# Optimization experiments

Hardware: AMD Instinct MI355X
Metric: run time of the kernel (lower is better)

Reference implementation:

```python
import jax, jax.numpy as jnp
import numpy as np

B, S, D, H, M, E, K = 4, 2048, 1024, 2048, 64, 8, 2  # batch, seq, d_model, max_neurons, moe_hidden, experts, top_k


def setup_inputs() -> dict:
    key = jax.random.key(0)
    ks = jax.random.split(key, 10)
    r = lambda k, shape: jax.random.normal(k, shape, dtype=jnp.float32) * 0.02
    return {
        "inputs_embeds": jax.random.normal(ks[0], (B, S, D), dtype=jnp.float32),
        "enc_W": r(ks[1], (D, H)), "enc_b": jnp.zeros((H,), jnp.float32),
        "s2c_W": r(ks[2], (H, M)), "s2c_b": jnp.zeros((M,), jnp.float32),
        "rW1": r(ks[3], (M, 64)), "rb1": jnp.zeros((64,), jnp.float32),
        "rW2": r(ks[4], (64, E)), "rb2": jnp.zeros((E,), jnp.float32),
        "We1": r(ks[5], (E, M, H // 2)), "be1": jnp.zeros((E, H // 2), jnp.float32),
        "We2": r(ks[6], (E, H // 2, M)), "be2": jnp.zeros((E, M), jnp.float32),
        "c2s_W": r(ks[7], (M, H)), "c2s_b": jnp.zeros((H,), jnp.float32),
        "dec_W": r(ks[8], (H, D)), "dec_b": jnp.zeros((D,), jnp.float32),
        "ln_g": jnp.ones((D,), jnp.float32), "ln_b": jnp.zeros((D,), jnp.float32),
    }


def _layernorm(x, g, b, eps=1e-5):
    mu = x.mean(-1, keepdims=True)
    var = ((x - mu) ** 2).mean(-1, keepdims=True)
    return (x - mu) * jax.lax.rsqrt(var + eps) * g + b


def _forward(inputs_embeds, enc_W, enc_b, s2c_W, s2c_b, rW1, rb1, rW2, rb2,
             We1, be1, We2, be2, c2s_W, c2s_b, dec_W, dec_b, ln_g, ln_b):
    b, s, _ = inputs_embeds.shape
    # GIFNeuron encoder (rate-coded surrogate spikes)
    spikes_enc = jax.nn.sigmoid(inputs_embeds @ enc_W + enc_b)          # (B,S,H)
    flat = spikes_enc.reshape(b * s, H)                                  # (N,H)
    # SpikeToContinuousBridge ('rate'): projection to MoE hidden
    cont = flat @ s2c_W + s2c_b                                          # (N,M)
    # LiquidMoERouter: 2-layer router, softmax, top-k, renormalize
    logits = jnp.tanh(cont @ rW1 + rb1) @ rW2 + rb2                      # (N,E)
    probs = jax.nn.softmax(logits, axis=-1)
    topw, topi = jax.lax.top_k(probs, K)                                 # (N,K)
    w = topw / topw.sum(-1, keepdims=True)
    # dense per-token per-expert gate == sum_k weights[:,k] * (indices[:,k]==e)
    gates = (jax.nn.one_hot(topi, E, dtype=cont.dtype) * w[..., None]).sum(1)  # (N,E)
    # SNNExpert MLP per expert, dense dispatch + weighted combine (index_add equivalent)
    h = jax.nn.relu(jnp.einsum('nm,emh->enh', cont, We1) + be1[:, None, :])    # (E,N,H/2)
    expert_out = jnp.einsum('enh,ehm->enm', h, We2) + be2[:, None, :]          # (E,N,M)
    output_flat = jnp.einsum('enm,ne->nm', expert_out, gates)                  # (N,M)
    # ContinuousToSpikeBridge ('poisson', expected rate), 2D -> 1 timestep
    spikes_moe = jax.nn.sigmoid(output_flat @ c2s_W + c2s_b).reshape(b, s, H)
    # GIFNeuron decoder + LayerNorm
    decoded = jax.nn.sigmoid(spikes_moe @ dec_W + dec_b)                 # (B,S,D)
    return _layernorm(decoded, ln_g, ln_b)


def reference(inputs_embeds, enc_W, enc_b, s2c_W, s2c_b, rW1, rb1, rW2, rb2,
              We1, be1, We2, be2, c2s_W, c2s_b, dec_W, dec_b, ln_g, ln_b):
    return _forward(inputs_embeds, enc_W, enc_b, s2c_W, s2c_b, rW1, rb1, rW2, rb2,
                    We1, be1, We2, be2, c2s_W, c2s_b, dec_W, dec_b, ln_g, ln_b)
```

## Files before the change

### kernel.cpp

```cpp
#include <hip/hip_runtime.h>
#include <hip/hip_bf16.h>
#include <cstdint>
#include <cstddef>

#define TOK    8192
#define DMODEL 1024
#define HDIM   2048
#define MDIM   64
#define NEXP   8
#define HHALF  1024

using f32x4  = __attribute__((ext_vector_type(4))) float;
using bf16x8 = __attribute__((ext_vector_type(8))) __bf16;
using bf16x4 = __attribute__((ext_vector_type(4))) __bf16;

__device__ __forceinline__ void async16(const void* g, void* l) {
  __builtin_amdgcn_global_load_lds(
      (const __attribute__((address_space(1))) unsigned int*)g,
      (__attribute__((address_space(3))) unsigned int*)l, 16, 0, 0);
}

__global__ __launch_bounds__(256) void preamble_kernel(
    const float* __restrict__ X, __bf16* __restrict__ Xb,
    const float* __restrict__ encW, __bf16* __restrict__ encWT,
    const float* __restrict__ s2cW, __bf16* __restrict__ s2cWT,
    const float* __restrict__ c2sW, __bf16* __restrict__ c2sWT,
    const float* __restrict__ decW, __bf16* __restrict__ decWT,
    const float* __restrict__ We1, __bf16* __restrict__ We1T,
    const float* __restrict__ We2, __bf16* __restrict__ We2T) {
  __shared__ float ts[32][33];
  const int tid = threadIdx.x;
  int b = blockIdx.x;
  if (b < 8192) {
    int i = b * 256 + tid;
    float4 v = ((const float4*)X)[i];
    bf16x4 o = { (__bf16)v.x, (__bf16)v.y, (__bf16)v.z, (__bf16)v.w };
    ((bf16x4*)Xb)[i] = o;
    return;
  }
  b -= 8192;
  const float* in; __bf16* outp; int R, C, tx, ty;
  if (b < 2048)              { in = encW; outp = encWT; R = 1024; C = 2048; tx = b % 64; ty = b / 64; }
  else if ((b -= 2048) < 128){ in = s2cW; outp = s2cWT; R = 2048; C = 64;   tx = b % 2;  ty = b / 2;  }
  else if ((b -= 128) < 128) { in = c2sW; outp = c2sWT; R = 64;   C = 2048; tx = b % 64; ty = b / 64; }
  else if ((b -= 128) < 2048){ in = decW; outp = decWT; R = 2048; C = 1024; tx = b % 32; ty = b / 32; }
  else if ((b -= 2048) < 512){ int s = b / 64, t = b % 64;
                               in = We1 + (size_t)s * 65536; outp = We1T + (size_t)s * 65536;
                               R = 64; C = 1024; tx = t % 32; ty = t / 32; }
  else                       { b -= 512; int s = b / 64, t = b % 64;
                               in = We2 + (size_t)s * 65536; outp = We2T + (size_t)s * 65536;
                               R = 1024; C = 64; tx = t % 2; ty = t / 2; }
  const int c0 = tx * 32, r0 = ty * 32;
  const int x = tid & 31, y = tid >> 5;
  #pragma unroll
  for (int i = y; i < 32; i += 8) ts[i][x] = in[(size_t)(r0 + i) * C + c0 + x];
  __syncthreads();
  #pragma unroll
  for (int i = y; i < 32; i += 8)
    outp[(size_t)(c0 + i) * R + r0 + x] = (__bf16)ts[x][i];
}
#define PREAMBLE_BLOCKS (8192 + 2048 + 128 + 128 + 2048 + 512 + 512)

template <int BN, int WAVES, int NBUF, int OUT_BF16, int ACT, int BIAS>
__global__ __launch_bounds__(WAVES * 64, 2) void gemm_mt(
    const __bf16* __restrict__ A, const __bf16* __restrict__ Bt,
    const float* __restrict__ bias, void* __restrict__ Cout,
    int M, int N, int K) {
  constexpr int BM = 256, BK = 64;
  constexpr int A_ISSUES = BM / (8 * WAVES);
  constexpr int B_ISSUES = BN / (8 * WAVES);
  constexpr int LOADS = A_ISSUES + B_ISSUES;
  static_assert(NBUF == 2 && LOADS == 8, "vmcnt literal assumes LOADS=8");
  __shared__ __bf16 As[NBUF * BM * BK];
  __shared__ __bf16 Bs[NBUF * BN * BK];
  const int tid = threadIdx.x;
  const int wave = tid >> 6, lane = tid & 63;
  const int quad = lane >> 4, l16 = lane & 15;
  const int m0 = blockIdx.x * BM, n0 = blockIdx.y * BN;
  const int wm = (wave & 1) * 128;
  const int wn = (wave >> 1) * 64;
  const int lrow = lane >> 3, lchunk = lane & 7;
  f32x4 acc[8][4] = {};

  const __bf16* aSrc[A_ISSUES];
  const __bf16* bSrc[B_ISSUES];
  #pragma unroll
  for (int t = 0; t < A_ISSUES; ++t) {
    int row = (t * WAVES + wave) * 8 + lrow;
    aSrc[t] = A + (size_t)(m0 + row) * K + (lchunk ^ (row & 7)) * 8;
  }
  #pragma unroll
  for (int t = 0; t < B_ISSUES; ++t) {
    int row = (t * WAVES + wave) * 8 + lrow;
    bSrc[t] = Bt + (size_t)(n0 + row) * K + (lchunk ^ (row & 7)) * 8;
  }
  int aOff[8], bOff[4];
  #pragma unroll
  for (int rf = 0; rf < 8; ++rf) {
    int row = wm + rf * 16 + l16;
    aOff[rf] = row * BK + ((quad ^ (row & 7)) * 8);
  }
  #pragma unroll
  for (int cf = 0; cf < 4; ++cf) {
    int row = wn + cf * 16 + l16;
    bOff[cf] = row * BK + ((quad ^ (row & 7)) * 8);
  }

  auto stage = [&](__bf16* Ad, __bf16* Bd) {
    #pragma unroll
    for (int t = 0; t < A_ISSUES; ++t) {
      async16(aSrc[t], Ad + (t * WAVES + wave) * 8 * BK);
      aSrc[t] += BK;
    }
    #pragma unroll
    for (int t = 0; t < B_ISSUES; ++t) {
      async16(bSrc[t], Bd + (t * WAVES + wave) * 8 * BK);
      bSrc[t] += BK;
    }
  };

  __bf16 *cA0 = As, *cA1 = As + BM * BK;
  __bf16 *cB0 = Bs, *cB1 = Bs + BN * BK;
  const int nt = K / BK;
  stage(cA0, cB0);

  for (int t = 0; t < nt; ++t) {
    if (t + 1 < nt) stage(cA1, cB1);
    if (t + 1 < nt) asm volatile("s_waitcnt vmcnt(8)" ::: "memory");
    else            asm volatile("s_waitcnt vmcnt(0)" ::: "memory");
    asm volatile("s_barrier" ::: "memory");

    bf16x8 af[4], ag[4], bv[4], bw[4];
    #pragma unroll
    for (int r = 0; r < 4; ++r) af[r] = *(const bf16x8*)(cA0 + aOff[r]);
    #pragma unroll
    for (int c = 0; c < 4; ++c) bv[c] = *(const bf16x8*)(cB0 + bOff[c]);
    #pragma unroll
    for (int r = 0; r < 4; ++r) ag[r] = *(const bf16x8*)(cA0 + aOff[4 + r]);
    __builtin_amdgcn_s_setprio(1);
    #pragma unroll
    for (int c = 0; c < 4; ++c)
      #pragma unroll
      for (int r = 0; r < 4; ++r)
        acc[r][c] = __builtin_amdgcn_mfma_f32_16x16x32_bf16(af[r], bv[c], acc[r][c], 0, 0, 0);
    __builtin_amdgcn_s_setprio(0);
    asm volatile("s_barrier" ::: "memory");
    #pragma unroll
    for (int r = 0; r < 4; ++r) af[r] = *(const bf16x8*)(cA0 + (aOff[r] ^ 32));
    #pragma unroll
    for (int c = 0; c < 4; ++c) bw[c] = *(const bf16x8*)(cB0 + (bOff[c] ^ 32));
    __builtin_amdgcn_s_setprio(1);
    #pragma unroll
    for (int c = 0; c < 4; ++c)
      #pragma unroll
      for (int r = 0; r < 4; ++r)
        acc[4 + r][c] = __builtin_amdgcn_mfma_f32_16x16x32_bf16(ag[r], bv[c], acc[4 + r][c], 0, 0, 0);
    __builtin_amdgcn_s_setprio(0);
    asm volatile("s_barrier" ::: "memory");
    #pragma unroll
    for (int r = 0; r < 4; ++r) ag[r] = *(const bf16x8*)(cA0 + (aOff[4 + r] ^ 32));
    __builtin_amdgcn_s_setprio(1);
    #pragma unroll
    for (int c = 0; c < 4; ++c)
      #pragma unroll
      for (int r = 0; r < 4; ++r)
        acc[r][c] = __builtin_amdgcn_mfma_f32_16x16x32_bf16(af[r], bw[c], acc[r][c], 0, 0, 0);
    __builtin_amdgcn_s_setprio(0);
    asm volatile("s_barrier" ::: "memory");
    __builtin_amdgcn_s_setprio(1);
    #pragma unroll
    for (int c = 0; c < 4; ++c)
      #pragma unroll
      for (int r = 0; r < 4; ++r)
        acc[4 + r][c] = __builtin_amdgcn_mfma_f32_16x16x32_bf16(ag[r], bw[c], acc[4 + r][c], 0, 0, 0);
    __builtin_amdgcn_s_setprio(0);
    asm volatile("s_barrier" ::: "memory");

    __bf16* x;
    x = cA0; cA0 = cA1; cA1 = x;
    x = cB0; cB0 = cB1; cB1 = x;
  }

  #pragma unroll
  for (int rf = 0; rf < 8; ++rf)
    #pragma unroll
    for (int cf = 0; cf < 4; ++cf)
      #pragma unroll
      for (int r = 0; r < 4; ++r) {
        int m = m0 + wm + rf * 16 + quad * 4 + r;
        int n = n0 + wn + cf * 16 + l16;
        float v = acc[rf][cf][r];
        if (BIAS) v += bias[n];
        if (ACT == 1) v = 1.0f / (1.0f + __expf(-v));
        if (OUT_BF16)
          ((__bf16*)Cout)[(size_t)m * N + n] = (__bf16)v;
        else
          ((float*)Cout)[(size_t)m * N + n] = v;
      }
}

template <int BM, int BN, int WAVES, int OUT_BF16, int ACT, int BIAS, int SUMA>
__global__ __launch_bounds__(WAVES * 64) void gemm_bt(
    const __bf16* __restrict__ A, const __bf16* __restrict__ Bt,
    const float* __restrict__ bias, void* __restrict__ Cout,
    int M, int N, int K, const __bf16* __restrict__ A2) {
  constexpr int BK = 64;
  constexpr int WAVES_N = WAVES / 2;
  constexpr int WTM = BM / 32;
  constexpr int WTN = BN / (WAVES_N * 16);
  constexpr int NBUF = SUMA ? 1 : 2;
  constexpr int A_ISSUES = BM / (8 * WAVES);
  constexpr int B_ISSUES = BN / (8 * WAVES);
  __shared__ __bf16 As[NBUF * BM * BK];
  __shared__ __bf16 Bs[NBUF * BN * BK];
  const int tid = threadIdx.x;
  const int wave = tid >> 6, lane = tid & 63;
  const int quad = lane >> 4, l16 = lane & 15;
  const int m0 = blockIdx.x * BM, n0 = blockIdx.y * BN;
  const int ks = K / gridDim.z;
  const int kbeg = blockIdx.z * ks;
  const int wm = (wave & 1) * (BM / 2);
  const int wn = (wave >> 1) * (BN / WAVES_N);
  const int lrow = lane >> 3;
  const int lchunk = lane & 7;
  f32x4 acc[WTM][WTN] = {};

  const __bf16* aSrc[A_ISSUES];
  const __bf16* bSrc[B_ISSUES];
  #pragma unroll
  for (int t = 0; t < A_ISSUES; ++t) {
    int row = (t * WAVES + wave) * 8 + lrow;
    aSrc[t] = A + (size_t)(m0 + row) * K + kbeg + (lchunk ^ (row & 7)) * 8;
  }
  #pragma unroll
  for (int t = 0; t < B_ISSUES; ++t) {
    int row = (t * WAVES + wave) * 8 + lrow;
    bSrc[t] = Bt + (size_t)(n0 + row) * K + kbeg + (lchunk ^ (row & 7)) * 8;
  }
  int aOff[WTM][2], bOff[WTN][2];
  #pragma unroll
  for (int i = 0; i < WTM; ++i) {
    int row = wm + i * 16 + l16;
    #pragma unroll
    for (int kk = 0; kk < 2; ++kk)
      aOff[i][kk] = row * BK + (((kk * 4 + quad) ^ (row & 7)) * 8);
  }
  #pragma unroll
  for (int j = 0; j < WTN; ++j) {
    int row = wn + j * 16 + l16;
    #pragma unroll
    for (int kk = 0; kk < 2; ++kk)
      bOff[j][kk] = row * BK + (((kk * 4 + quad) ^ (row & 7)) * 8);
  }

  auto stage = [&](__bf16* Ad, __bf16* Bd) {
    #pragma unroll
    for (int t = 0; t < A_ISSUES; ++t) {
      async16(aSrc[t], Ad + (t * WAVES + wave) * 8 * BK);
      aSrc[t] += BK;
    }
    #pragma unroll
    for (int t = 0; t < B_ISSUES; ++t) {
      async16(bSrc[t], Bd + (t * WAVES + wave) * 8 * BK);
      bSrc[t] += BK;
    }
  };
  auto compute = [&](const __bf16* Ab, const __bf16* Bb) {
    #pragma unroll
    for (int kk = 0; kk < 2; ++kk) {
      bf16x8 af[WTM], bfr[WTN];
      #pragma unroll
      for (int i = 0; i < WTM; ++i) af[i] = *(const bf16x8*)(Ab + aOff[i][kk]);
      #pragma unroll
      for (int j = 0; j < WTN; ++j) bfr[j] = *(const bf16x8*)(Bb + bOff[j][kk]);
      #pragma unroll
      for (int i = 0; i < WTM; ++i)
        #pragma unroll
        for (int j = 0; j < WTN; ++j)
          acc[i][j] = __builtin_amdgcn_mfma_f32_16x16x32_bf16(af[i], bfr[j], acc[i][j], 0, 0, 0);
    }
  };

  const int niter = ks / BK;
  if constexpr (SUMA) {
    for (int it = 0; it < niter; ++it) {
      __syncthreads();
      #pragma unroll
      for (int t = 0; t < A_ISSUES; ++t) {
        int row = (t * WAVES + wave) * 8 + lrow;
        size_t go = (size_t)(m0 + row) * K + kbeg + it * BK + lchunk * 8;
        bf16x8 a0 = *(const bf16x8*)(A + go);
        bf16x8 a1 = *(const bf16x8*)(A2 + go);
        bf16x8 s;
        #pragma unroll
        for (int q = 0; q < 8; ++q) s[q] = (__bf16)((float)a0[q] + (float)a1[q]);
        *(bf16x8*)(As + row * BK + ((lchunk ^ (row & 7)) * 8)) = s;
      }
      #pragma unroll
      for (int t = 0; t < B_ISSUES; ++t) {
        async16(bSrc[t], Bs + (t * WAVES + wave) * 8 * BK);
        bSrc[t] += BK;
      }
      __syncthreads();
      compute(As, Bs);
    }
  } else {
    __bf16* curA = As;  __bf16* nxtA = As + BM * BK;
    __bf16* curB = Bs;  __bf16* nxtB = Bs + BN * BK;
    stage(curA, curB);
    asm volatile("s_waitcnt vmcnt(0)" ::: "memory");
    __builtin_amdgcn_s_barrier();
    for (int it = 0; it < niter - 1; ++it) {
      stage(nxtA, nxtB);
      compute(curA, curB);
      asm volatile("s_waitcnt vmcnt(0)" ::: "memory");
      __builtin_amdgcn_s_barrier();
      { __bf16* t = curA; curA = nxtA; nxtA = t; }
      { __bf16* t = curB; curB = nxtB; nxtB = t; }
    }
    compute(curA, curB);
  }

  char* Cz = (char*)Cout + (size_t)blockIdx.z * M * N * (OUT_BF16 ? 2 : 4);
  #pragma unroll
  for (int i = 0; i < WTM; ++i)
    #pragma unroll
    for (int j = 0; j < WTN; ++j)
      #pragma unroll
      for (int r = 0; r < 4; ++r) {
        int m = m0 + wm + i * 16 + quad * 4 + r;
        int n = n0 + wn + j * 16 + l16;
        float v = acc[i][j][r];
        if (BIAS) v += bias[n];
        if (ACT == 1) v = 1.0f / (1.0f + __expf(-v));
        if (OUT_BF16)
          ((__bf16*)Cz)[(size_t)m * N + n] = (__bf16)v;
        else
          ((float*)Cz)[(size_t)m * N + n] = v;
      }
}

__global__ __launch_bounds__(256) void router_kernel(
    const float* __restrict__ contP, const float* __restrict__ s2c_b,
    const float* __restrict__ rW1, const float* __restrict__ rb1,
    const float* __restrict__ rW2, const float* __restrict__ rb2,
    __bf16* __restrict__ contB, int* __restrict__ e01,
    float2* __restrict__ g01, int* __restrict__ cnt) {
  if (blockIdx.x == 0 && threadIdx.x < NEXP) cnt[threadIdx.x] = 0;
  const int wave = threadIdx.x >> 6, lane = threadIdx.x & 63;
  const int n = blockIdx.x * 4 + wave;
  const size_t base = (size_t)n * 64 + lane;
  const size_t slab = (size_t)TOK * 64;
  float c = contP[base] + contP[base + slab] + contP[base + 2 * slab] +
            contP[base + 3 * slab] + s2c_b[lane];
  contB[base] = (__bf16)c;
  float acc = rb1[lane];
  #pragma unroll
  for (int i = 0; i < 64; ++i) {
    float ci = __shfl(c, i);
    acc = fmaf(ci, rW1[i * 64 + lane], acc);
  }
  float t = tanhf(acc);
  float logit[8];
  #pragma unroll
  for (int e = 0; e < 8; ++e) {
    float v = t * rW2[lane * 8 + e];
    #pragma unroll
    for (int o = 32; o; o >>= 1) v += __shfl_xor(v, o);
    logit[e] = v + rb2[e];
  }
  float mx = logit[0];
  #pragma unroll
  for (int e = 1; e < 8; ++e) mx = fmaxf(mx, logit[e]);
  float p[8];
  #pragma unroll
  for (int e = 0; e < 8; ++e) p[e] = __expf(logit[e] - mx);
  float v0 = p[0]; int e0 = 0;
  #pragma unroll
  for (int e = 1; e < 8; ++e) if (p[e] > v0) { v0 = p[e]; e0 = e; }
  float v1 = -1.0f; int e1 = 0;
  #pragma unroll
  for (int e = 0; e < 8; ++e) if (e != e0 && p[e] > v1) { v1 = p[e]; e1 = e; }
  float inv = 1.0f / (v0 + v1);
  if (lane == 0) {
    e01[n] = e0 | (e1 << 8);
    g01[n] = make_float2(v0 * inv, v1 * inv);
  }
}

__global__ __launch_bounds__(256) void fill_kernel(
    const int* __restrict__ e01, int* __restrict__ cnt,
    unsigned* __restrict__ idxb) {
  __shared__ int lcnt[NEXP], lbase[NEXP];
  const int tid = threadIdx.x;
  if (tid < NEXP) lcnt[tid] = 0;
  __syncthreads();
  const int n = blockIdx.x * 256 + tid;
  const int pe = e01[n];
  const int e0 = pe & 0xff, e1 = (pe >> 8) & 0xff;
  const int p0 = atomicAdd(&lcnt[e0], 1);
  const int p1 = atomicAdd(&lcnt[e1], 1);
  __syncthreads();
  if (tid < NEXP) lbase[tid] = atomicAdd(&cnt[tid], lcnt[tid]);
  __syncthreads();
  idxb[e0 * TOK + lbase[e0] + p0] = (unsigned)n;
  idxb[e1 * TOK + lbase[e1] + p1] = (unsigned)n | 0x80000000u;
}

__global__ __launch_bounds__(256) void moe_sparse_kernel(
    const __bf16* __restrict__ contB, const __bf16* __restrict__ We1T,
    const __bf16* __restrict__ We2T, const float* __restrict__ be1,
    const float* __restrict__ be2, const unsigned* __restrict__ idxb,
    const int* __restrict__ cnt, const float2* __restrict__ g01,
    __bf16* __restrict__ slab0, __bf16* __restrict__ slab1) {
  constexpr int TT = 64;
  const int e = blockIdx.y;
  const int start = blockIdx.x * TT;
  const int ne = cnt[e];
  if (start >= ne) return;
  const int nval = min(TT, ne - start);
  __shared__ __bf16 cont_s[TT * 64];
  __shared__ __bf16 w1_s[64 * 64];
  __shared__ __bf16 w2_s[64 * 64];
  __shared__ __bf16 h_s[TT * 64];
  __shared__ unsigned tok_s[TT];
  __shared__ float gate_s[TT];
  const int tid = threadIdx.x;
  const int wave = tid >> 6, lane = tid & 63;
  const int quad = lane >> 4, l16 = lane & 15;
  if (tid < TT) {
    unsigned v = idxb[e * TOK + start + ((tid < nval) ? tid : 0)];
    unsigned tok = v & 0x7fffffffu;
    float2 g = g01[tok];
    tok_s[tid] = v;
    gate_s[tid] = (v >> 31) ? g.y : g.x;
  }
  __syncthreads();
  for (int i = tid; i < TT * 8; i += 256) {
    int r = i >> 3, cc = i & 7;
    unsigned tok = tok_s[r] & 0x7fffffffu;
    *(uint4*)(cont_s + r * 64 + ((cc ^ (r & 7)) * 8)) =
        *(const uint4*)(contB + (size_t)tok * 64 + cc * 8);
  }
  const int wtok = wave * 16;
  f32x4 acc2[4] = {};
  for (int hc = 0; hc < HHALF; hc += 64) {
    __syncthreads();
    for (int c = tid; c < 512; c += 256) {
      int r = c >> 3, cc = c & 7;
      *(uint4*)(w1_s + r * 64 + ((cc ^ (r & 7)) * 8)) =
          *(const uint4*)(We1T + ((size_t)e * HHALF + hc + r) * 64 + cc * 8);
      *(uint4*)(w2_s + r * 64 + ((cc ^ (r & 7)) * 8)) =
          *(const uint4*)(We2T + ((size_t)e * 64 + r) * HHALF + hc + cc * 8);
    }
    __syncthreads();
    f32x4 acc1[4] = {};
    #pragma unroll
    for (int kk = 0; kk < 2; ++kk) {
      bf16x8 af, bfr[4];
      {
        int row = wtok + l16;
        af = *(const bf16x8*)(cont_s + row * 64 + (((kk * 4 + quad) ^ (row & 7)) * 8));
      }
      #pragma unroll
      for (int j = 0; j < 4; ++j) {
        int row = j * 16 + l16;
        bfr[j] = *(const bf16x8*)(w1_s + row * 64 + (((kk * 4 + quad) ^ (row & 7)) * 8));
      }
      #pragma unroll
      for (int j = 0; j < 4; ++j)
        acc1[j] = __builtin_amdgcn_mfma_f32_16x16x32_bf16(af, bfr[j], acc1[j], 0, 0, 0);
    }
    #pragma unroll
    for (int j = 0; j < 4; ++j)
      #pragma unroll
      for (int r = 0; r < 4; ++r) {
        int tr = wtok + quad * 4 + r;
        int hcol = j * 16 + l16;
        float v = acc1[j][r] + be1[e * HHALF + hc + hcol];
        h_s[tr * 64 + (((hcol >> 3) ^ (tr & 7)) * 8) + (hcol & 7)] =
            (__bf16)fmaxf(v, 0.0f);
      }
    #pragma unroll
    for (int kk = 0; kk < 2; ++kk) {
      bf16x8 af, bfr[4];
      {
        int row = wtok + l16;
        af = *(const bf16x8*)(h_s + row * 64 + (((kk * 4 + quad) ^ (row & 7)) * 8));
      }
      #pragma unroll
      for (int j = 0; j < 4; ++j) {
        int row = j * 16 + l16;
        bfr[j] = *(const bf16x8*)(w2_s + row * 64 + (((kk * 4 + quad) ^ (row & 7)) * 8));
      }
      #pragma unroll
      for (int j = 0; j < 4; ++j)
        acc2[j] = __builtin_amdgcn_mfma_f32_16x16x32_bf16(af, bfr[j], acc2[j], 0, 0, 0);
    }
  }
  #pragma unroll
  for (int j = 0; j < 4; ++j)
    #pragma unroll
    for (int r = 0; r < 4; ++r) {
      int tr = wtok + quad * 4 + r;
      if (tr < nval) {
        unsigned v = tok_s[tr];
        unsigned tok = v & 0x7fffffffu;
        int m = j * 16 + l16;
        float o = gate_s[tr] * (acc2[j][r] + be2[e * 64 + m]);
        __bf16* slab = (v >> 31) ? slab1 : slab0;
        slab[(size_t)tok * 64 + m] = (__bf16)o;
      }
    }
}

__global__ __launch_bounds__(256) void ln_kernel(
    const float* __restrict__ x, const float* __restrict__ g,
    const float* __restrict__ b, float* __restrict__ out) {
  const int row = blockIdx.x;
  const float4 v = ((const float4*)(x + (size_t)row * 1024))[threadIdx.x];
  float s1 = v.x + v.y + v.z + v.w;
  float s2 = v.x * v.x + v.y * v.y + v.z * v.z + v.w * v.w;
  #pragma unroll
  for (int o = 32; o; o >>= 1) { s1 += __shfl_xor(s1, o); s2 += __shfl_xor(s2, o); }
  __shared__ float ws1[4], ws2[4];
  const int wave = threadIdx.x >> 6, lane = threadIdx.x & 63;
  if (lane == 0) { ws1[wave] = s1; ws2[wave] = s2; }
  __syncthreads();
  s1 = ws1[0] + ws1[1] + ws1[2] + ws1[3];
  s2 = ws2[0] + ws2[1] + ws2[2] + ws2[3];
  const float mu = s1 * (1.0f / 1024.0f);
  const float var = s2 * (1.0f / 1024.0f) - mu * mu;
  const float inv = rsqrtf(var + 1e-5f);
  const int col = threadIdx.x * 4;
  const float4 gv = *(const float4*)(g + col);
  const float4 bv = *(const float4*)(b + col);
  float4 o;
  o.x = (v.x - mu) * inv * gv.x + bv.x;
  o.y = (v.y - mu) * inv * gv.y + bv.y;
  o.z = (v.z - mu) * inv * gv.z + bv.z;
  o.w = (v.w - mu) * inv * gv.w + bv.w;
  *(float4*)(out + (size_t)row * 1024 + col) = o;
}

extern "C" void kernel_launch(void* const* d_in, const int* in_sizes, int n_in,
                              void* d_out, int out_size, void* d_ws, size_t ws_size,
                              hipStream_t stream) {
  const float* X     = (const float*)d_in[0];
  const float* enc_W = (const float*)d_in[1];
  const float* enc_b = (const float*)d_in[2];
  const float* s2c_W = (const float*)d_in[3];
  const float* s2c_b = (const float*)d_in[4];
  const float* rW1   = (const float*)d_in[5];
  const float* rb1   = (const float*)d_in[6];
  const float* rW2   = (const float*)d_in[7];
  const float* rb2   = (const float*)d_in[8];
  const float* We1   = (const float*)d_in[9];
  const float* be1   = (const float*)d_in[10];
  const float* We2   = (const float*)d_in[11];
  const float* be2   = (const float*)d_in[12];
  const float* c2s_W = (const float*)d_in[13];
  const float* c2s_b = (const float*)d_in[14];
  const float* dec_W = (const float*)d_in[15];
  const float* dec_b = (const float*)d_in[16];
  const float* ln_g  = (const float*)d_in[17];
  const float* ln_b  = (const float*)d_in[18];
  float* out = (float*)d_out;

  char* ws = (char*)d_ws;
  size_t off = 0;
  auto take = [&](size_t bytes) -> char* {
    char* p = ws + off;
    off = (off + bytes + 255) & ~(size_t)255;
    return p;
  };
  const size_t SLAB = (size_t)TOK * HDIM * 2;
  char*   slabA     = take(SLAB);
  char*   slabB     = take(SLAB);
  __bf16* encWT     = (__bf16*)take((size_t)HDIM * DMODEL * 2);
  __bf16* s2cWT     = (__bf16*)take((size_t)MDIM * HDIM * 2);
  __bf16* c2sWT     = (__bf16*)take((size_t)HDIM * MDIM * 2);
  __bf16* decWT     = (__bf16*)take((size_t)DMODEL * HDIM * 2);
  __bf16* We1T      = (__bf16*)take((size_t)NEXP * HHALF * MDIM * 2);
  __bf16* We2T      = (__bf16*)take((size_t)NEXP * MDIM * HHALF * 2);
  __bf16* contB     = (__bf16*)take((size_t)TOK * MDIM * 2);
  int*    e01       = (int*)take((size_t)TOK * 4);
  float2* g01       = (float2*)take((size_t)TOK * 8);
  __bf16* oslab0    = (__bf16*)take((size_t)TOK * MDIM * 2);
  __bf16* oslab1    = (__bf16*)take((size_t)TOK * MDIM * 2);
  int*     cnt      = (int*)take((size_t)NEXP * 4);
  unsigned* idxb    = (unsigned*)take((size_t)NEXP * TOK * 4);
  if (off > ws_size) return;

  __bf16* Xb        = (__bf16*)slabA;
  float*  contP     = (float*)(slabA + (size_t)TOK * DMODEL * 2);
  __bf16* spikesMoe = (__bf16*)slabA;
  __bf16* spikesEnc = (__bf16*)slabB;
  float*  decoded   = (float*)slabB;

  preamble_kernel<<<PREAMBLE_BLOCKS, 256, 0, stream>>>(
      X, Xb, enc_W, encWT, s2c_W, s2cWT, c2s_W, c2sWT, dec_W, decWT,
      We1, We1T, We2, We2T);

  gemm_mt<256, 8, 2, 1, 1, 1><<<dim3(TOK / 256, HDIM / 256), 512, 0, stream>>>(
      Xb, encWT, enc_b, spikesEnc, TOK, HDIM, DMODEL);
  gemm_bt<128, 64, 4, 0, 0, 0, 0><<<dim3(TOK / 128, 1, 4), 256, 0, stream>>>(
      spikesEnc, s2cWT, nullptr, contP, TOK, MDIM, HDIM, nullptr);
  router_kernel<<<TOK / 4, 256, 0, stream>>>(contP, s2c_b, rW1, rb1, rW2, rb2,
                                             contB, e01, g01, cnt);
  fill_kernel<<<TOK / 256, 256, 0, stream>>>(e01, cnt, idxb);
  moe_sparse_kernel<<<dim3(TOK / 64, NEXP), 256, 0, stream>>>(
      contB, We1T, We2T, be1, be2, idxb, cnt, g01, oslab0, oslab1);
  gemm_bt<128, 128, 4, 1, 1, 1, 1><<<dim3(TOK / 128, HDIM / 128, 1), 256, 0, stream>>>(
      oslab0, c2sWT, c2s_b, spikesMoe, TOK, HDIM, MDIM, oslab1);
  gemm_bt<128, 128, 4, 0, 1, 1, 0><<<dim3(TOK / 128, DMODEL / 128, 1), 256, 0, stream>>>(
      spikesMoe, decWT, dec_b, decoded, TOK, DMODEL, HDIM, nullptr);
  ln_kernel<<<TOK, 256, 0, stream>>>(decoded, ln_g, ln_b, out);
}
```

Before: 311.7 us.

## Interleave next-tile async loads across MFMA phases and reuse kernel for decoder GEMM

The 8-wave 256-row GEMM now issues the next K-tile's global-to-LDS loads in chunks between the four MFMA phases instead of all at once at the top of each iteration. The goal is to overlap memory traffic with compute and smooth out VMEM issue. The kernel is generalized to BN=128 and also used for the decoder GEMM, which replaces the 128x128 4-wave gemm_bt. This adds scheduling barriers and hand-tuned vmcnt waits whose correctness depends on the exact load counts per phase.

```diff
diff --git a/kernel.cpp b/kernel.cpp
--- a/kernel.cpp
+++ b/kernel.cpp
@@ -61,130 +61,161 @@
 }
 #define PREAMBLE_BLOCKS (8192 + 2048 + 128 + 128 + 2048 + 512 + 512)
 
-template <int BN, int WAVES, int NBUF, int OUT_BF16, int ACT, int BIAS>
-__global__ __launch_bounds__(WAVES * 64, 2) void gemm_mt(
+template <int BN, int OUT_BF16, int ACT, int BIAS>
+__global__ __launch_bounds__(512, 2) void gemm_8p(
     const __bf16* __restrict__ A, const __bf16* __restrict__ Bt,
     const float* __restrict__ bias, void* __restrict__ Cout,
     int M, int N, int K) {
   constexpr int BM = 256, BK = 64;
-  constexpr int A_ISSUES = BM / (8 * WAVES);
-  constexpr int B_ISSUES = BN / (8 * WAVES);
-  constexpr int LOADS = A_ISSUES + B_ISSUES;
-  static_assert(NBUF == 2 && LOADS == 8, "vmcnt literal assumes LOADS=8");
-  __shared__ __bf16 As[NBUF * BM * BK];
-  __shared__ __bf16 Bs[NBUF * BN * BK];
+  constexpr int WTN = BN / 64;
+  constexpr int A_LOADS = 4;
+  constexpr int B_LOADS = BN / 64;
+  __shared__ __bf16 As[2 * BM * BK];
+  __shared__ __bf16 Bs[2 * BN * BK];
   const int tid = threadIdx.x;
   const int wave = tid >> 6, lane = tid & 63;
   const int quad = lane >> 4, l16 = lane & 15;
   const int m0 = blockIdx.x * BM, n0 = blockIdx.y * BN;
   const int wm = (wave & 1) * 128;
-  const int wn = (wave >> 1) * 64;
+  const int wn = (wave >> 1) * (BN / 4);
   const int lrow = lane >> 3, lchunk = lane & 7;
-  f32x4 acc[8][4] = {};
-
-  const __bf16* aSrc[A_ISSUES];
-  const __bf16* bSrc[B_ISSUES];
-  #pragma unroll
-  for (int t = 0; t < A_ISSUES; ++t) {
-    int row = (t * WAVES + wave) * 8 + lrow;
+  f32x4 acc[8][WTN] = {};
+
+  const __bf16* aSrc[A_LOADS];
+  const __bf16* bSrc[B_LOADS];
+  #pragma unroll
+  for (int t = 0; t < A_LOADS; ++t) {
+    int row = (t * 8 + wave) * 8 + lrow;
     aSrc[t] = A + (size_t)(m0 + row) * K + (lchunk ^ (row & 7)) * 8;
   }
   #pragma unroll
-  for (int t = 0; t < B_ISSUES; ++t) {
-    int row = (t * WAVES + wave) * 8 + lrow;
+  for (int t = 0; t < B_LOADS; ++t) {
+    int row = (t * 8 + wave) * 8 + lrow;
     bSrc[t] = Bt + (size_t)(n0 + row) * K + (lchunk ^ (row & 7)) * 8;
   }
-  int aOff[8], bOff[4];
+  int aOff[8], bOff[WTN];
   #pragma unroll
   for (int rf = 0; rf < 8; ++rf) {
     int row = wm + rf * 16 + l16;
     aOff[rf] = row * BK + ((quad ^ (row & 7)) * 8);
   }
   #pragma unroll
-  for (int cf = 0; cf < 4; ++cf) {
+  for (int cf = 0; cf < WTN; ++cf) {
     int row = wn + cf * 16 + l16;
     bOff[cf] = row * BK + ((quad ^ (row & 7)) * 8);
   }
 
-  auto stage = [&](__bf16* Ad, __bf16* Bd) {
-    #pragma unroll
-    for (int t = 0; t < A_ISSUES; ++t) {
-      async16(aSrc[t], Ad + (t * WAVES + wave) * 8 * BK);
-      aSrc[t] += BK;
-    }
-    #pragma unroll
-    for (int t = 0; t < B_ISSUES; ++t) {
-      async16(bSrc[t], Bd + (t * WAVES + wave) * 8 * BK);
-      bSrc[t] += BK;
-    }
+  auto stageA = [&](int t, __bf16* Ad) {
+    async16(aSrc[t], Ad + (t * 8 + wave) * 8 * BK);
+    aSrc[t] += BK;
   };
-
-  __bf16 *cA0 = As, *cA1 = As + BM * BK;
-  __bf16 *cB0 = Bs, *cB1 = Bs + BN * BK;
+  auto stageB = [&](int t, __bf16* Bd) {
+    async16(bSrc[t], Bd + (t * 8 + wave) * 8 * BK);
+    bSrc[t] += BK;
+  };
+
+  __bf16 *curA = As, *nxtA = As + BM * BK;
+  __bf16 *curB = Bs, *nxtB = Bs + BN * BK;
   const int nt = K / BK;
-  stage(cA0, cB0);
+
+  stageB(0, curB); stageB(1, curB);
+  if constexpr (BN == 256) { stageB(2, curB); stageB(3, curB); }
+  stageA(0, curA); stageA(2, curA);
+  stageA(1, curA); stageA(3, curA);
+  asm volatile("s_waitcnt vmcnt(0)" ::: "memory");
+  __builtin_amdgcn_s_barrier();
 
   for (int t = 0; t < nt; ++t) {
-    if (t + 1 < nt) stage(cA1, cB1);
-    if (t + 1 < nt) asm volatile("s_waitcnt vmcnt(8)" ::: "memory");
-    else            asm volatile("s_waitcnt vmcnt(0)" ::: "memory");
-    asm volatile("s_barrier" ::: "memory");
-
-    bf16x8 af[4], ag[4], bv[4], bw[4];
-    #pragma unroll
-    for (int r = 0; r < 4; ++r) af[r] = *(const bf16x8*)(cA0 + aOff[r]);
-    #pragma unroll
-    for (int c = 0; c < 4; ++c) bv[c] = *(const bf16x8*)(cB0 + bOff[c]);
-    #pragma unroll
-    for (int r = 0; r < 4; ++r) ag[r] = *(const bf16x8*)(cA0 + aOff[4 + r]);
+    const bool pre = (t + 1 < nt);
+    bf16x8 af[4], bv[WTN];
+    #pragma unroll
+    for (int r = 0; r < 4; ++r) af[r] = *(const bf16x8*)(curA + aOff[r]);
+    #pragma unroll
+    for (int c = 0; c < WTN; ++c) bv[c] = *(const bf16x8*)(curB + bOff[c]);
+    if (pre) {
+      stageB(0, nxtB); stageB(1, nxtB);
+      asm volatile("s_waitcnt vmcnt(2)" ::: "memory");
+    } else {
+      asm volatile("s_waitcnt vmcnt(0)" ::: "memory");
+    }
+    __builtin_amdgcn_s_barrier();
+    __builtin_amdgcn_sched_barrier(0);
     __builtin_amdgcn_s_setprio(1);
     #pragma unroll
-    for (int c = 0; c < 4; ++c)
+    for (int c = 0; c < WTN; ++c)
       #pragma unroll
       for (int r = 0; r < 4; ++r)
         acc[r][c] = __builtin_amdgcn_mfma_f32_16x16x32_bf16(af[r], bv[c], acc[r][c], 0, 0, 0);
     __builtin_amdgcn_s_setprio(0);
-    asm volatile("s_barrier" ::: "memory");
-    #pragma unroll
-    for (int r = 0; r < 4; ++r) af[r] = *(const bf16x8*)(cA0 + (aOff[r] ^ 32));
-    #pragma unroll
-    for (int c = 0; c < 4; ++c) bw[c] = *(const bf16x8*)(cB0 + (bOff[c] ^ 32));
+    __builtin_amdgcn_s_barrier();
+    bf16x8 ag[4];
+    #pragma unroll
+    for (int r = 0; r < 4; ++r) ag[r] = *(const bf16x8*)(curA + aOff[4 + r]);
+    if (pre) {
+      if constexpr (BN == 256) { stageB(2, nxtB); stageB(3, nxtB); }
+      else                     { stageA(0, nxtA); stageA(2, nxtA); }
+    }
+    __builtin_amdgcn_s_barrier();
+    __builtin_amdgcn_sched_barrier(0);
     __builtin_amdgcn_s_setprio(1);
     #pragma unroll
-    for (int c = 0; c < 4; ++c)
+    for (int c = 0; c < WTN; ++c)
       #pragma unroll
       for (int r = 0; r < 4; ++r)
         acc[4 + r][c] = __builtin_amdgcn_mfma_f32_16x16x32_bf16(ag[r], bv[c], acc[4 + r][c], 0, 0, 0);
     __builtin_amdgcn_s_setprio(0);
-    asm volatile("s_barrier" ::: "memory");
-    #pragma unroll
-    for (int r = 0; r < 4; ++r) ag[r] = *(const bf16x8*)(cA0 + (aOff[4 + r] ^ 32));
+    __builtin_amdgcn_s_barrier();
+    bf16x8 af2[4], bw[WTN];
+    #pragma unroll
+    for (int r = 0; r < 4; ++r) af2[r] = *(const bf16x8*)(curA + (aOff[r] ^ 32));
+    #pragma unroll
+    for (int c = 0; c < WTN; ++c) bw[c] = *(const bf16x8*)(curB + (bOff[c] ^ 32));
+    if (pre) {
+      if constexpr (BN == 256) { stageA(0, nxtA); stageA(2, nxtA); }
+      else {
+        stageA(1, nxtA); stageA(3, nxtA);
+        asm volatile("s_waitcnt vmcnt(2)" ::: "memory");
+      }
+    }
+    __builtin_amdgcn_s_barrier();
+    __builtin_amdgcn_sched_barrier(0);
     __builtin_amdgcn_s_setprio(1);
     #pragma unroll
-    for (int c = 0; c < 4; ++c)
+    for (int c = 0; c < WTN; ++c)
       #pragma unroll
       for (int r = 0; r < 4; ++r)
-        acc[r][c] = __builtin_amdgcn_mfma_f32_16x16x32_bf16(af[r], bw[c], acc[r][c], 0, 0, 0);
+        acc[r][c] = __builtin_amdgcn_mfma_f32_16x16x32_bf16(af2[r], bw[c], acc[r][c], 0, 0, 0);
     __builtin_amdgcn_s_setprio(0);
-    asm volatile("s_barrier" ::: "memory");
+    __builtin_amdgcn_s_barrier();
+    bf16x8 ag2[4];
+    #pragma unroll
+    for (int r = 0; r < 4; ++r) ag2[r] = *(const bf16x8*)(curA + (aOff[4 + r] ^ 32));
+    if (pre) {
+      if constexpr (BN == 256) {
+        stageA(1, nxtA); stageA(3, nxtA);
+        asm volatile("s_waitcnt vmcnt(2)" ::: "memory");
+      }
+    }
+    __builtin_amdgcn_s_barrier();
+    __builtin_amdgcn_sched_barrier(0);
     __builtin_amdgcn_s_setprio(1);
     #pragma unroll
-    for (int c = 0; c < 4; ++c)
+    for (int c = 0; c < WTN; ++c)
       #pragma unroll
       for (int r = 0; r < 4; ++r)
-        acc[4 + r][c] = __builtin_amdgcn_mfma_f32_16x16x32_bf16(ag[r], bw[c], acc[4 + r][c], 0, 0, 0);
+        acc[4 + r][c] = __builtin_amdgcn_mfma_f32_16x16x32_bf16(ag2[r], bw[c], acc[4 + r][c], 0, 0, 0);
     __builtin_amdgcn_s_setprio(0);
-    asm volatile("s_barrier" ::: "memory");
+    __builtin_amdgcn_s_barrier();
 
     __bf16* x;
-    x = cA0; cA0 = cA1; cA1 = x;
-    x = cB0; cB0 = cB1; cB1 = x;
+    x = curA; curA = nxtA; nxtA = x;
+    x = curB; curB = nxtB; nxtB = x;
   }
 
   #pragma unroll
   for (int rf = 0; rf < 8; ++rf)
     #pragma unroll
-    for (int cf = 0; cf < 4; ++cf)
+    for (int cf = 0; cf < WTN; ++cf)
       #pragma unroll
       for (int r = 0; r < 4; ++r) {
         int m = m0 + wm + rf * 16 + quad * 4 + r;
@@ -602,7 +633,7 @@
       X, Xb, enc_W, encWT, s2c_W, s2cWT, c2s_W, c2sWT, dec_W, decWT,
       We1, We1T, We2, We2T);
 
-  gemm_mt<256, 8, 2, 1, 1, 1><<<dim3(TOK / 256, HDIM / 256), 512, 0, stream>>>(
+  gemm_8p<256, 1, 1, 1><<<dim3(TOK / 256, HDIM / 256), 512, 0, stream>>>(
       Xb, encWT, enc_b, spikesEnc, TOK, HDIM, DMODEL);
   gemm_bt<128, 64, 4, 0, 0, 0, 0><<<dim3(TOK / 128, 1, 4), 256, 0, stream>>>(
       spikesEnc, s2cWT, nullptr, contP, TOK, MDIM, HDIM, nullptr);
@@ -613,7 +644,7 @@
       contB, We1T, We2T, be1, be2, idxb, cnt, g01, oslab0, oslab1);
   gemm_bt<128, 128, 4, 1, 1, 1, 1><<<dim3(TOK / 128, HDIM / 128, 1), 256, 0, stream>>>(
       oslab0, c2sWT, c2s_b, spikesMoe, TOK, HDIM, MDIM, oslab1);
-  gemm_bt<128, 128, 4, 0, 1, 1, 0><<<dim3(TOK / 128, DMODEL / 128, 1), 256, 0, stream>>>(
-      spikesMoe, decWT, dec_b, decoded, TOK, DMODEL, HDIM, nullptr);
+  gemm_8p<128, 0, 1, 1><<<dim3(TOK / 256, DMODEL / 128), 512, 0, stream>>>(
+      spikesMoe, decWT, dec_b, decoded, TOK, DMODEL, HDIM);
   ln_kernel<<<TOK, 256, 0, stream>>>(decoded, ln_g, ln_b, out);
 }
```

Result: faster. 304.7 us (-2.2%).
